# Performance work log

Measured on AMD Instinct MI355X. Metric: run time of the kernel, lower is better.

The kernel has to match this reference:

```python
import jax, jax.numpy as jnp
import numpy as np
import math
from functools import lru_cache

DIM = 64   # num_inputs
HID = 32   # hidden_dim
B = 1024
LOG2 = math.log(2.0)
LOG_2PI = math.log(2.0 * math.pi)


@lru_cache(maxsize=None)
def _masks(out_f, in_f, dim):
    ob, ib = out_f // dim, in_f // dim
    md = np.zeros((out_f, in_f), np.float32)
    mo = np.ones((out_f, in_f), np.float32)
    for i in range(dim):
        md[i * ob:(i + 1) * ob, i * ib:(i + 1) * ib] = 1.0
        mo[i * ob:(i + 1) * ob, i * ib:] = 0.0
    return jnp.asarray(md), jnp.asarray(mo)


def masked_weight(x, grad, W, dw, b, dim):
    # W: (out_f, in_f), dw: (out_f, 1), b: (out_f,)
    out_f, in_f = W.shape
    ob, ib = out_f // dim, in_f // dim
    md, mo = _masks(out_f, in_f, dim)
    w = jnp.exp(W) * md + W * mo                      # positive diag blocks, masked lower blocks
    wsn = jnp.sum(w * w, axis=-1, keepdims=True)      # (out_f, 1) weight-norm denom^2
    wn = jnp.exp(dw) * w / jnp.sqrt(wsn)              # weight-normalized matrix
    wpl = dw + W - 0.5 * jnp.log(wsn)                 # log of diag-block entries, (out_f, in_f)
    # extract diagonal blocks: (dim, ob, dim, ib) -> diag over block index -> (ob, ib, dim)
    blocks = jnp.diagonal(wpl.reshape(dim, ob, dim, ib), axis1=0, axis2=2)
    g = jnp.transpose(blocks, (2, 0, 1))              # (dim, ob, ib) == torch g per-sample
    out = x @ wn.T + b
    if grad is None:
        return out, jnp.broadcast_to(g[None], (x.shape[0],) + g.shape)
    # grad: (Bt, dim, a, c); log-domain block 'matmul' via logsumexp over shared axis a(=ib)
    comb = g[None, :, :, None, :] + jnp.swapaxes(grad, -1, -2)[:, :, None, :, :]  # (Bt,dim,ob,c,ib)
    return out, jax.nn.logsumexp(comb, axis=-1)       # (Bt, dim, ob, c)


def tanh_layer(x, grad):
    g = -2.0 * (x - LOG2 + jax.nn.softplus(-2.0 * x))
    return jnp.tanh(x), g.reshape(grad.shape) + grad


def bnaf_flow(x, p0, p1, p2, gate, dim):
    out, grad = masked_weight(x, None, *p0, dim)
    out, grad = tanh_layer(out, grad)
    out, grad = masked_weight(out, grad, *p1, dim)
    out, grad = tanh_layer(out, grad)
    out, grad = masked_weight(out, grad, *p2, dim)
    g = grad.reshape(grad.shape[0], dim)              # squeeze (B, dim, 1, 1) -> (B, dim)
    if gate is None:
        return out, jnp.sum(g, -1)
    s = jax.nn.sigmoid(gate)
    out = s * out + (1.0 - s) * x
    ldj = jnp.sum(jax.nn.softplus(g + gate) - jax.nn.softplus(gate), -1)
    return out, ldj


def _forward(x, params, gates):
    ldj = 0.0
    for f in range(3):
        gate = gates[f] if f < 2 else None
        x, l = bnaf_flow(x, params[f][0], params[f][1], params[f][2], gate, DIM)
        ldj = ldj + l
        if f < 2:
            x = x[:, ::-1]                            # Permutation('flip'), log-det 0
    log_p_y = jnp.sum(-0.5 * x * x - 0.5 * LOG_2PI, -1)
    return log_p_y + ldj                              # (B,)


def setup_inputs() -> dict:
    key = jax.random.key(0)
    ks = iter(jax.random.split(key, 64))
    d, dh = DIM, DIM * HID
    shapes = [(dh, d), (dh, dh), (d, dh)]
    inp = {"x": jax.random.normal(next(ks), (B, d), jnp.float32)}
    for f in range(3):
        for l, (o, i) in enumerate(shapes):
            inp[f"W{f}_{l}"] = 0.1 * jax.random.normal(next(ks), (o, i), jnp.float32)
            inp[f"dw{f}_{l}"] = jnp.log(jax.random.uniform(next(ks), (o, 1), jnp.float32, 0.1, 1.0))
            inp[f"b{f}_{l}"] = 0.01 * jax.random.normal(next(ks), (o,), jnp.float32)
    inp["gate0"] = jax.random.normal(next(ks), (1,), jnp.float32)
    inp["gate1"] = jax.random.normal(next(ks), (1,), jnp.float32)
    return inp


def reference(x, W0_0, dw0_0, b0_0, W0_1, dw0_1, b0_1, W0_2, dw0_2, b0_2,
              W1_0, dw1_0, b1_0, W1_1, dw1_1, b1_1, W1_2, dw1_2, b1_2,
              W2_0, dw2_0, b2_0, W2_1, dw2_1, b2_1, W2_2, dw2_2, b2_2,
              gate0, gate1):
    params = [
        [(W0_0, dw0_0, b0_0), (W0_1, dw0_1, b0_1), (W0_2, dw0_2, b0_2)],
        [(W1_0, dw1_0, b1_0), (W1_1, dw1_1, b1_1), (W1_2, dw1_2, b1_2)],
        [(W2_0, dw2_0, b2_0), (W2_1, dw2_1, b2_1), (W2_2, dw2_2, b2_2)],
    ]
    return _forward(x, params, (gate0, gate1))
```

## Files before the change

kernel.cpp:

```cpp
#include <hip/hip_runtime.h>
#include <hip/hip_bf16.h>
#include <math.h>


#define DIMN 64
#define BATCH 1024
#define HIDF 2048
#define SPLITK 4
#define NT2 32

typedef __attribute__((ext_vector_type(8))) short short8;
typedef __attribute__((ext_vector_type(4))) float floatx4;

__device__ __forceinline__ float softplusf_(float t) {
    return fmaxf(t, 0.f) + log1pf(__expf(-fabsf(t)));
}

__device__ __forceinline__ float bf2f(short v) {
    union { unsigned u; float f; } x;
    x.u = ((unsigned)(unsigned short)v) << 16;
    return x.f;
}

__device__ __forceinline__ void gl_lds16(const void* g, void* l) {
    __builtin_amdgcn_global_load_lds(
        (const __attribute__((address_space(1))) unsigned int*)g,
        (__attribute__((address_space(3))) unsigned int*)l, 16, 0, 0);
}

__device__ __forceinline__ void tanh_sech2_(float p, float& th, float& s2) {
    float t = __expf(-2.f * fabsf(p));
    float opt = 1.f + t;
    float inv = 1.f / opt;
    th = copysignf((1.f - t) * inv, p);
    s2 = 4.f * t * inv * inv;
}

template<int INF>
__device__ __forceinline__ void prep_row(
    const float* __restrict__ W, const float* __restrict__ dw,
    void* __restrict__ wn_out, float* __restrict__ eg,
    int r, int lane, int out_f, int ob, int ib, int transpose, int bf16out)
{
    constexpr int NI = INF / 64;
    int d = r / ob;
    int c0 = d * ib;
    int c1 = c0 + ib;
    const float* Wr = W + (size_t)r * INF;

    float vv[NI];
    float ss = 0.f;
#pragma unroll
    for (int i = 0; i < NI; ++i) {
        int c = lane + i * 64;
        float wraw = Wr[c];
        float wv = (c < c0) ? wraw : ((c < c1) ? __expf(wraw) : 0.f);
        vv[i] = wv;
        ss += wv * wv;
    }
    for (int off = 32; off > 0; off >>= 1) ss += __shfl_xor(ss, off, 64);

    float dwr = dw[r];
    float scale = __expf(dwr) / sqrtf(ss);
    float logt = dwr - 0.5f * __logf(ss);

#pragma unroll
    for (int i = 0; i < NI; ++i) {
        int c = lane + i * 64;
        float val = scale * vv[i];
        if (bf16out) {
            ((__hip_bfloat16*)wn_out)[(size_t)r * INF + c] = __float2bfloat16(val);
        } else if (transpose) {
            ((float*)wn_out)[(size_t)c * out_f + r] = val;
        } else {
            ((float*)wn_out)[(size_t)r * INF + c] = val;
        }
    }
    if (lane < ib) eg[(size_t)r * ib + lane] = __expf(logt + Wr[c0 + lane]);
}

struct PrepIn { const float *W0, *dw0, *W1, *dw1, *W2, *dw2; };

__global__ __launch_bounds__(64) void prep_mega(
    PrepIn p0, PrepIn p1, PrepIn p2,
    float* __restrict__ wn0T_all, float* __restrict__ eg0_all,
    __hip_bfloat16* __restrict__ wn1_all, float* __restrict__ e1_all,
    __hip_bfloat16* __restrict__ wn2b_all, float* __restrict__ e2_all)
{
    int blk = blockIdx.x;
    int lane = threadIdx.x;
    int f = blk / 4160;
    int rem = blk - f * 4160;
    PrepIn P = (f == 0) ? p0 : ((f == 1) ? p1 : p2);

    float* wn0T = wn0T_all + (size_t)f * DIMN * HIDF;
    float* eg0  = eg0_all  + (size_t)f * HIDF;
    __hip_bfloat16* wn1 = wn1_all + (size_t)f * HIDF * HIDF;
    float* e1   = e1_all   + (size_t)f * HIDF * 32;
    __hip_bfloat16* wn2b = wn2b_all + (size_t)f * DIMN * HIDF;
    float* e2   = e2_all   + (size_t)f * DIMN * 32;

    if (rem < HIDF) {
        prep_row<DIMN>(P.W0, P.dw0, wn0T, eg0, rem, lane, HIDF, 32, 1, 1, 0);
    } else if (rem < 2 * HIDF) {
        prep_row<HIDF>(P.W1, P.dw1, wn1, e1, rem - HIDF, lane, HIDF, 32, 32, 0, 1);
    } else {
        prep_row<HIDF>(P.W2, P.dw2, wn2b, e2, rem - 2 * HIDF, lane, DIMN, 1, 32, 0, 1);
    }
}

__global__ __launch_bounds__(256) void gemm0_act(
    const float* __restrict__ xin, const float* __restrict__ wn0T,
    const float* __restrict__ bias, const float* __restrict__ eg0,
    __hip_bfloat16* __restrict__ h0, __hip_bfloat16* __restrict__ g0e)
{
    __shared__ float xs[16][DIMN];
    int b0 = blockIdx.y * 16;
    {
        const float4* src = (const float4*)(xin + (size_t)b0 * DIMN);
        ((float4*)xs)[threadIdx.x] = src[threadIdx.x];
    }
    __syncthreads();
    int n = blockIdx.x * 256 + threadIdx.x;

    float acc[16];
#pragma unroll
    for (int j = 0; j < 16; ++j) acc[j] = 0.f;

#pragma unroll 4
    for (int c4 = 0; c4 < 16; ++c4) {
        int c = c4 * 4;
        float w0 = wn0T[(size_t)(c + 0) * HIDF + n];
        float w1 = wn0T[(size_t)(c + 1) * HIDF + n];
        float w2 = wn0T[(size_t)(c + 2) * HIDF + n];
        float w3 = wn0T[(size_t)(c + 3) * HIDF + n];
#pragma unroll
        for (int j = 0; j < 16; ++j) {
            float4 x4 = *(const float4*)&xs[j][c];
            acc[j] = fmaf(x4.x, w0, acc[j]);
            acc[j] = fmaf(x4.y, w1, acc[j]);
            acc[j] = fmaf(x4.z, w2, acc[j]);
            acc[j] = fmaf(x4.w, w3, acc[j]);
        }
    }
    float bv = bias[n], egv = eg0[n];
#pragma unroll
    for (int j = 0; j < 16; ++j) {
        float p = acc[j] + bv;
        float th, s2;
        tanh_sech2_(p, th, s2);
        size_t idx = (size_t)(b0 + j) * HIDF + n;
        h0[idx] = __float2bfloat16(th);
        g0e[idx] = __float2bfloat16(egv * s2);
    }
}

__constant__ unsigned char G1_JN[40] = {
    3,4,5,6,7,7,8,8,9,9,10,10,11,11,11,12,12,12,13,13,13,14,14,14,
    15,15,15,15, 2,6,10,14, 1,5,9,13, 0,4,8,12 };
__constant__ unsigned char G1_KZ[40] = {
    0,0,0,0,0,1,0,1,0,1, 0, 1, 0, 1, 2, 0, 1, 2, 0, 1, 2, 0, 1, 2,
     0, 1, 2, 3, 0,1, 2, 3, 0,1,2,3, 0,1,2,3 };

#define G1BK 64
__global__ __launch_bounds__(256) void gemm1_part(
    const __hip_bfloat16* __restrict__ A, const __hip_bfloat16* __restrict__ B,
    __hip_bfloat16* __restrict__ part)
{
    const int K = HIDF, N = HIDF;
    int pr = blockIdx.x >> 3;
    int my = blockIdx.x & 7;
    int jn = G1_JN[pr];
    int kz = G1_KZ[pr];
    int kbase = kz * (K / SPLITK);
    int kend = (jn + 1) * 128 - kbase;
    if (kend > K / SPLITK) kend = K / SPLITK;

    __shared__ short As[128 * 64];
    __shared__ short Bs[128 * 64];
    int tid = threadIdx.x;
    int lane = tid & 63;
    int wave = tid >> 6;
    int n0 = jn * 128;
    int m0 = my * 128;
    int wr = wave >> 1;
    int wc = wave & 1;

    int rf = lane & 15;
    int q = lane >> 4;

    const char* agp[4];
    const char* bgp[4];
    char* alds[4];
    char* blds[4];
#pragma unroll
    for (int s = 0; s < 4; ++s) {
        int c = tid + s * 256;
        int row = c >> 3;
        int kc = (c & 7) ^ (row & 7);
        agp[s] = (const char*)A + ((size_t)(m0 + row) * K + kbase) * 2 + kc * 16;
        bgp[s] = (const char*)B + ((size_t)(n0 + row) * K + kbase) * 2 + kc * 16;
        alds[s] = (char*)As + c * 16;
        blds[s] = (char*)Bs + c * 16;
    }

    floatx4 acc[4][4];
#pragma unroll
    for (int i = 0; i < 4; ++i)
#pragma unroll
        for (int j = 0; j < 4; ++j) acc[i][j] = (floatx4){0.f, 0.f, 0.f, 0.f};

    int rowA0 = wr * 64 + rf;
    int rowB0 = wc * 64 + rf;

    for (int k0 = 0; k0 < kend; k0 += G1BK) {
        size_t kb = (size_t)k0 * 2;
        __syncthreads();
#pragma unroll
        for (int s = 0; s < 4; ++s) {
            gl_lds16(agp[s] + kb, alds[s]);
            gl_lds16(bgp[s] + kb, blds[s]);
        }
        __syncthreads();

#pragma unroll
        for (int s = 0; s < 2; ++s) {
            short8 af[4], bfv[4];
#pragma unroll
            for (int i = 0; i < 4; ++i) {
                int row = rowA0 + i * 16;
                af[i] = *(const short8*)&As[row * 64 + (((s * 4 + q) ^ (row & 7)) * 8)];
            }
#pragma unroll
            for (int j = 0; j < 4; ++j) {
                int row = rowB0 + j * 16;
                bfv[j] = *(const short8*)&Bs[row * 64 + (((s * 4 + q) ^ (row & 7)) * 8)];
            }
#pragma unroll
            for (int i = 0; i < 4; ++i)
#pragma unroll
                for (int j = 0; j < 4; ++j)
                    acc[i][j] = __builtin_amdgcn_mfma_f32_16x16x32_bf16(af[i], bfv[j], acc[i][j], 0, 0, 0);
        }
    }

    __hip_bfloat16* pk = part + (size_t)kz * BATCH * HIDF;
    int col = lane & 15;
    int rq = (lane >> 4) * 4;
#pragma unroll
    for (int i = 0; i < 4; ++i) {
#pragma unroll
        for (int j = 0; j < 4; ++j) {
            int n = n0 + wc * 64 + j * 16 + col;
#pragma unroll
            for (int r = 0; r < 4; ++r) {
                int m = m0 + wr * 64 + i * 16 + rq + r;
                pk[(size_t)m * N + n] = __float2bfloat16(acc[i][j][r]);
            }
        }
    }
}

__global__ __launch_bounds__(256) void act_grad_gemm2(
    const __hip_bfloat16* __restrict__ part, const float* __restrict__ bias,
    const float* __restrict__ e1, const __hip_bfloat16* __restrict__ g0e,
    const __hip_bfloat16* __restrict__ wn2b,
    __hip_bfloat16* __restrict__ grad1e, float* __restrict__ out2p)
{
    __shared__ char smem[17408 + 8704 + 8192];
    float* g0s = (float*)smem;
    short* h1s = (short*)(smem + 17408);
    short* Bs2 = (short*)(smem + 17408 + 8704);

    int tid = threadIdx.x;
    int lane = tid & 63;
    int wave = tid >> 6;
    int bx = blockIdx.x;
    int n0 = bx * 64;
    int b0 = blockIdx.y * 64;
    int np = (bx >> 3) + 1;

    {
        int c0c = tid, c1c = tid + 256;
        int r0 = c0c >> 3, k0c = (c0c & 7) ^ (r0 & 7);
        int r1 = c1c >> 3, k1c = (c1c & 7) ^ (r1 & 7);
        gl_lds16((const char*)wn2b + ((size_t)r0 * HIDF + n0) * 2 + k0c * 16,
                 (char*)Bs2 + c0c * 16);
        gl_lds16((const char*)wn2b + ((size_t)r1 * HIDF + n0) * 2 + k1c * 16,
                 (char*)Bs2 + c1c * 16);
    }

    for (int s = tid; s < 512; s += 256) {
        int row = s >> 3, c8 = s & 7;
        short8 v = *(const short8*)((const short*)g0e +
                                    (size_t)(b0 + row) * HIDF + n0 + c8 * 8);
        float4 lo = { bf2f(v[0]), bf2f(v[1]), bf2f(v[2]), bf2f(v[3]) };
        float4 hi = { bf2f(v[4]), bf2f(v[5]), bf2f(v[6]), bf2f(v[7]) };
        *(float4*)&g0s[row * 68 + c8 * 8] = lo;
        *(float4*)&g0s[row * 68 + c8 * 8 + 4] = hi;
    }

    int g = tid >> 6;
    int nl = tid & 63;
    int n = n0 + nl;

    float4 er[8];
    const float4* e1r = (const float4*)(e1 + (size_t)n * 32);
#pragma unroll
    for (int qq = 0; qq < 8; ++qq) er[qq] = e1r[qq];

    float bv = bias[n];
    int kb2 = nl & 32;
    const __hip_bfloat16* pp0 = part;
    const __hip_bfloat16* pp1 = (np > 1) ? part + (size_t)1 * BATCH * HIDF : part;
    const __hip_bfloat16* pp2 = (np > 2) ? part + (size_t)2 * BATCH * HIDF : part;
    const __hip_bfloat16* pp3 = (np > 3) ? part + (size_t)3 * BATCH * HIDF : part;
    float m1 = (np > 1) ? 1.f : 0.f;
    float m2 = (np > 2) ? 1.f : 0.f;
    float m3 = (np > 3) ? 1.f : 0.f;

    __syncthreads();

#pragma unroll
    for (int t = 0; t < 16; ++t) {
        int bl = g * 16 + t;
        int b = b0 + bl;
        size_t idx = (size_t)b * HIDF + n;
        float l0 = __bfloat162float(pp0[idx]);
        float l1 = __bfloat162float(pp1[idx]);
        float l2 = __bfloat162float(pp2[idx]);
        float l3 = __bfloat162float(pp3[idx]);
        float pre = bv + l0;
        pre = fmaf(m1, l1, pre);
        pre = fmaf(m2, l2, pre);
        pre = fmaf(m3, l3, pre);
        float th, s2;
        tanh_sech2_(pre, th, s2);
        const float* g0row = &g0s[bl * 68 + kb2];
        float dot = 0.f;
#pragma unroll
        for (int qq = 0; qq < 8; ++qq) {
            float4 gv = *(const float4*)&g0row[qq * 4];
            dot = fmaf(gv.x, er[qq].x, dot);
            dot = fmaf(gv.y, er[qq].y, dot);
            dot = fmaf(gv.z, er[qq].z, dot);
            dot = fmaf(gv.w, er[qq].w, dot);
        }
        __hip_bfloat16 thb = __float2bfloat16(th);
        h1s[bl * 68 + nl] = *(const short*)&thb;
        grad1e[idx] = __float2bfloat16(dot * s2);
    }
    __syncthreads();

    int rf = lane & 15;
    int q = lane >> 4;
    floatx4 acc2[4];
#pragma unroll
    for (int j = 0; j < 4; ++j) acc2[j] = (floatx4){0.f, 0.f, 0.f, 0.f};

#pragma unroll
    for (int s = 0; s < 2; ++s) {
        int rowa = wave * 16 + rf;
        short8 af = *(const short8*)&h1s[rowa * 68 + s * 32 + q * 8];
#pragma unroll
        for (int j = 0; j < 4; ++j) {
            int rowb = j * 16 + rf;
            int cp = (s * 4 + q) ^ (rowb & 7);
            short8 bfv = *(const short8*)&Bs2[rowb * 64 + cp * 8];
            acc2[j] = __builtin_amdgcn_mfma_f32_16x16x32_bf16(af, bfv, acc2[j], 0, 0, 0);
        }
    }

    float* outk = out2p + (size_t)bx * BATCH * DIMN;
    int col = lane & 15;
    int rq = (lane >> 4) * 4;
#pragma unroll
    for (int j = 0; j < 4; ++j) {
#pragma unroll
        for (int r = 0; r < 4; ++r) {
            int m = b0 + wave * 16 + rq + r;
            outk[(size_t)m * DIMN + j * 16 + col] = acc2[j][r];
        }
    }
}

__global__ __launch_bounds__(256) void tail_trans(
    const float* __restrict__ out2p, const float* __restrict__ b2,
    const float* __restrict__ e2, const __hip_bfloat16* __restrict__ grad1e,
    const float* __restrict__ x_cur, const float* __restrict__ gate,
    float* __restrict__ x_next, float* __restrict__ ldj, int accum_ldj)
{
    int tid = threadIdx.x;
    int b = blockIdx.x * 4 + (tid >> 6);
    int n = tid & 63;

    float o = b2[n];
#pragma unroll
    for (int p = 0; p < NT2; ++p)
        o += out2p[(size_t)p * BATCH * DIMN + (size_t)b * DIMN + n];

    float gt = gate[0];
    float sg = 1.f / (1.f + __expf(-gt));
    float xo = sg * o + (1.f - sg) * x_cur[(size_t)b * DIMN + n];
    x_next[(size_t)b * DIMN + (63 - n)] = xo;

    const short8* gr = (const short8*)((const short*)grad1e + (size_t)b * HIDF + n * 32);
    const float4* gc = (const float4*)(e2 + n * 32);
    float s = 0.f;
#pragma unroll
    for (int q = 0; q < 4; ++q) {
        short8 a8 = gr[q];
        float4 c0 = gc[2 * q], c1 = gc[2 * q + 1];
        s = fmaf(bf2f(a8[0]), c0.x, s);
        s = fmaf(bf2f(a8[1]), c0.y, s);
        s = fmaf(bf2f(a8[2]), c0.z, s);
        s = fmaf(bf2f(a8[3]), c0.w, s);
        s = fmaf(bf2f(a8[4]), c1.x, s);
        s = fmaf(bf2f(a8[5]), c1.y, s);
        s = fmaf(bf2f(a8[6]), c1.z, s);
        s = fmaf(bf2f(a8[7]), c1.w, s);
    }
    float gF = __logf(fmaxf(s, 1e-45f));
    float contrib = softplusf_(gF + gt) - softplusf_(gt);
    for (int off = 32; off > 0; off >>= 1) contrib += __shfl_xor(contrib, off, 64);
    if (n == 0) ldj[b] = accum_ldj ? (ldj[b] + contrib) : contrib;
}

__global__ __launch_bounds__(256) void tail_final(
    const float* __restrict__ out2p, const float* __restrict__ b2,
    const float* __restrict__ e2, const __hip_bfloat16* __restrict__ grad1e,
    const float* __restrict__ ldj, float* __restrict__ out)
{
    int tid = threadIdx.x;
    int b = blockIdx.x * 4 + (tid >> 6);
    int n = tid & 63;

    float o = b2[n];
#pragma unroll
    for (int p = 0; p < NT2; ++p)
        o += out2p[(size_t)p * BATCH * DIMN + (size_t)b * DIMN + n];

    const short8* gr = (const short8*)((const short*)grad1e + (size_t)b * HIDF + n * 32);
    const float4* gc = (const float4*)(e2 + n * 32);
    float s = 0.f;
#pragma unroll
    for (int q = 0; q < 4; ++q) {
        short8 a8 = gr[q];
        float4 c0 = gc[2 * q], c1 = gc[2 * q + 1];
        s = fmaf(bf2f(a8[0]), c0.x, s);
        s = fmaf(bf2f(a8[1]), c0.y, s);
        s = fmaf(bf2f(a8[2]), c0.z, s);
        s = fmaf(bf2f(a8[3]), c0.w, s);
        s = fmaf(bf2f(a8[4]), c1.x, s);
        s = fmaf(bf2f(a8[5]), c1.y, s);
        s = fmaf(bf2f(a8[6]), c1.z, s);
        s = fmaf(bf2f(a8[7]), c1.w, s);
    }
    float gF = __logf(fmaxf(s, 1e-45f));

    float contrib = gF - 0.5f * o * o - 0.91893853320467274f;
    for (int off = 32; off > 0; off >>= 1) contrib += __shfl_xor(contrib, off, 64);
    if (n == 0) out[b] = ldj[b] + contrib;
}

extern "C" void kernel_launch(void* const* d_in, const int* in_sizes, int n_in,
                              void* d_out, int out_size, void* d_ws, size_t ws_size,
                              hipStream_t stream)
{
    (void)in_sizes; (void)n_in; (void)out_size; (void)ws_size;

    const float* x = (const float*)d_in[0];
    const float* gates[2] = { (const float*)d_in[28], (const float*)d_in[29] };

    char* ws = (char*)d_ws;
    size_t ofs = 0;
    auto alloc = [&](size_t bytes) { char* p = ws + ofs; ofs += (bytes + 255) & ~(size_t)255; return p; };

    __hip_bfloat16* wn1_all  = (__hip_bfloat16*)alloc((size_t)3 * HIDF * HIDF * 2);
    __hip_bfloat16* wn2b_all = (__hip_bfloat16*)alloc((size_t)3 * DIMN * HIDF * 2);
    float* wn0T_all = (float*)alloc((size_t)3 * DIMN * HIDF * 4);
    float* eg0_all  = (float*)alloc((size_t)3 * HIDF * 4);
    float* e1_all   = (float*)alloc((size_t)3 * HIDF * 32 * 4);
    float* e2_all   = (float*)alloc((size_t)3 * DIMN * 32 * 4);
    __hip_bfloat16* h0   = (__hip_bfloat16*)alloc((size_t)BATCH * HIDF * 2);
    __hip_bfloat16* part = (__hip_bfloat16*)alloc((size_t)SPLITK * BATCH * HIDF * 2);
    __hip_bfloat16* g0e    = (__hip_bfloat16*)alloc((size_t)BATCH * HIDF * 2);
    __hip_bfloat16* grad1e = (__hip_bfloat16*)alloc((size_t)BATCH * HIDF * 2);
    float* out2p  = (float*)alloc((size_t)NT2 * BATCH * DIMN * 4);
    float* x1     = (float*)alloc((size_t)BATCH * DIMN * 4);
    float* x2     = (float*)alloc((size_t)BATCH * DIMN * 4);
    float* ldj    = (float*)alloc(BATCH * 4);
    float* outp   = (float*)d_out;

    auto W = [&](int f, int i) { return (const float*)d_in[1 + f * 9 + i]; };

    PrepIn p0 = { W(0,0), W(0,1), W(0,3), W(0,4), W(0,6), W(0,7) };
    PrepIn p1 = { W(1,0), W(1,1), W(1,3), W(1,4), W(1,6), W(1,7) };
    PrepIn p2 = { W(2,0), W(2,1), W(2,3), W(2,4), W(2,6), W(2,7) };

    prep_mega<<<dim3(3 * 4160), dim3(64), 0, stream>>>(
        p0, p1, p2, wn0T_all, eg0_all, wn1_all, e1_all, wn2b_all, e2_all);

    gemm0_act<<<dim3(8, BATCH / 16), dim3(256), 0, stream>>>(
        x, wn0T_all, W(0,2), eg0_all, h0, g0e);

    const float* xcur = x;
    float* xnexts[2] = { x1, x2 };

    for (int f = 0; f < 3; ++f) {
        size_t fo1 = (size_t)f * HIDF * HIDF;
        size_t fo2 = (size_t)f * DIMN * HIDF;

        gemm1_part<<<dim3(320), dim3(256), 0, stream>>>(
            h0, wn1_all + fo1, part);

        act_grad_gemm2<<<dim3(HIDF / 64, BATCH / 64), dim3(256), 0, stream>>>(
            part, W(f,5), e1_all + (size_t)f * HIDF * 32, g0e,
            wn2b_all + fo2, grad1e, out2p);

        if (f < 2) {
            tail_trans<<<dim3(BATCH / 4), dim3(256), 0, stream>>>(
                out2p, W(f,8), e2_all + (size_t)f * DIMN * 32, grad1e,
                xcur, gates[f], xnexts[f], ldj, f);

            gemm0_act<<<dim3(8, BATCH / 16), dim3(256), 0, stream>>>(
                xnexts[f], wn0T_all + (size_t)(f + 1) * DIMN * HIDF, W(f + 1, 2),
                eg0_all + (size_t)(f + 1) * HIDF, h0, g0e);

            xcur = xnexts[f];
        } else {
            tail_final<<<dim3(BATCH / 4), dim3(256), 0, stream>>>(
                out2p, W(2,8), e2_all + (size_t)2 * DIMN * 32, grad1e, ldj, outp);
        }
    }
}
```

Baseline: 291.4 us.

## Double-buffer LDS loads in gemm1 and fuse next-flow gemm0 into tail kernel

gemm1_part now keeps two LDS stages, so the global-to-LDS copy for the next K tile is issued while MFMAs run on the current tile, and only one barrier is needed per iteration. Separately, the tail kernel for flows 0 and 1 now also computes the next flow's first layer (x @ wn0T, tanh, gradient) from an LDS copy of the new x, which removes the separate gemm0_act launch. LDS per gemm1 block doubles to 64 KB, which may lower occupancy. The fused gemm0 runs on only 4 batch rows per block and re-reads the full wn0T in each of 256 blocks, so it reuses weights far less than the old 16-row kernel.

```diff
diff --git a/kernel.cpp b/kernel.cpp
--- a/kernel.cpp
+++ b/kernel.cpp
@@ -11,6 +11,7 @@
 
 typedef __attribute__((ext_vector_type(8))) short short8;
 typedef __attribute__((ext_vector_type(4))) float floatx4;
+typedef __hip_bfloat16 bf16;
 
 __device__ __forceinline__ float softplusf_(float t) {
     return fmaxf(t, 0.f) + log1pf(__expf(-fabsf(t)));
@@ -69,7 +70,7 @@
         int c = lane + i * 64;
         float val = scale * vv[i];
         if (bf16out) {
-            ((__hip_bfloat16*)wn_out)[(size_t)r * INF + c] = __float2bfloat16(val);
+            ((bf16*)wn_out)[(size_t)r * INF + c] = __float2bfloat16(val);
         } else if (transpose) {
             ((float*)wn_out)[(size_t)c * out_f + r] = val;
         } else {
@@ -84,8 +85,8 @@
 __global__ __launch_bounds__(64) void prep_mega(
     PrepIn p0, PrepIn p1, PrepIn p2,
     float* __restrict__ wn0T_all, float* __restrict__ eg0_all,
-    __hip_bfloat16* __restrict__ wn1_all, float* __restrict__ e1_all,
-    __hip_bfloat16* __restrict__ wn2b_all, float* __restrict__ e2_all)
+    bf16* __restrict__ wn1_all, float* __restrict__ e1_all,
+    bf16* __restrict__ wn2b_all, float* __restrict__ e2_all)
 {
     int blk = blockIdx.x;
     int lane = threadIdx.x;
@@ -95,9 +96,9 @@
 
     float* wn0T = wn0T_all + (size_t)f * DIMN * HIDF;
     float* eg0  = eg0_all  + (size_t)f * HIDF;
-    __hip_bfloat16* wn1 = wn1_all + (size_t)f * HIDF * HIDF;
+    bf16* wn1   = wn1_all + (size_t)f * HIDF * HIDF;
     float* e1   = e1_all   + (size_t)f * HIDF * 32;
-    __hip_bfloat16* wn2b = wn2b_all + (size_t)f * DIMN * HIDF;
+    bf16* wn2b  = wn2b_all + (size_t)f * DIMN * HIDF;
     float* e2   = e2_all   + (size_t)f * DIMN * 32;
 
     if (rem < HIDF) {
@@ -112,7 +113,7 @@
 __global__ __launch_bounds__(256) void gemm0_act(
     const float* __restrict__ xin, const float* __restrict__ wn0T,
     const float* __restrict__ bias, const float* __restrict__ eg0,
-    __hip_bfloat16* __restrict__ h0, __hip_bfloat16* __restrict__ g0e)
+    bf16* __restrict__ h0, bf16* __restrict__ g0e)
 {
     __shared__ float xs[16][DIMN];
     int b0 = blockIdx.y * 16;
@@ -164,9 +165,10 @@
 
 #define G1BK 64
 __global__ __launch_bounds__(256) void gemm1_part(
-    const __hip_bfloat16* __restrict__ A, const __hip_bfloat16* __restrict__ B,
-    __hip_bfloat16* __restrict__ part)
-{
+    const bf16* __restrict__ A, const bf16* __restrict__ B,
+    bf16* __restrict__ part)
+{
+    __shared__ __align__(16) char smem_[65536];
     const int K = HIDF, N = HIDF;
     int pr = blockIdx.x >> 3;
     int my = blockIdx.x & 7;
@@ -176,8 +178,6 @@
     int kend = (jn + 1) * 128 - kbase;
     if (kend > K / SPLITK) kend = K / SPLITK;
 
-    __shared__ short As[128 * 64];
-    __shared__ short Bs[128 * 64];
     int tid = threadIdx.x;
     int lane = tid & 63;
     int wave = tid >> 6;
@@ -185,14 +185,12 @@
     int m0 = my * 128;
     int wr = wave >> 1;
     int wc = wave & 1;
-
     int rf = lane & 15;
     int q = lane >> 4;
 
     const char* agp[4];
     const char* bgp[4];
-    char* alds[4];
-    char* blds[4];
+    int lofs[4];
 #pragma unroll
     for (int s = 0; s < 4; ++s) {
         int c = tid + s * 256;
@@ -200,8 +198,7 @@
         int kc = (c & 7) ^ (row & 7);
         agp[s] = (const char*)A + ((size_t)(m0 + row) * K + kbase) * 2 + kc * 16;
         bgp[s] = (const char*)B + ((size_t)(n0 + row) * K + kbase) * 2 + kc * 16;
-        alds[s] = (char*)As + c * 16;
-        blds[s] = (char*)Bs + c * 16;
+        lofs[s] = c * 16;
     }
 
     floatx4 acc[4][4];
@@ -213,16 +210,31 @@
     int rowA0 = wr * 64 + rf;
     int rowB0 = wc * 64 + rf;
 
+    {
+        char* base = smem_;
+#pragma unroll
+        for (int s = 0; s < 4; ++s) {
+            gl_lds16(agp[s], base + lofs[s]);
+            gl_lds16(bgp[s], base + 16384 + lofs[s]);
+        }
+    }
+    __syncthreads();
+
+    int cur = 0;
     for (int k0 = 0; k0 < kend; k0 += G1BK) {
-        size_t kb = (size_t)k0 * 2;
-        __syncthreads();
-#pragma unroll
-        for (int s = 0; s < 4; ++s) {
-            gl_lds16(agp[s] + kb, alds[s]);
-            gl_lds16(bgp[s] + kb, blds[s]);
-        }
-        __syncthreads();
-
+        int nk = k0 + G1BK;
+        if (nk < kend) {
+            size_t kb = (size_t)nk * 2;
+            char* base = smem_ + (cur ^ 1) * 32768;
+#pragma unroll
+            for (int s = 0; s < 4; ++s) {
+                gl_lds16(agp[s] + kb, base + lofs[s]);
+                gl_lds16(bgp[s] + kb, base + 16384 + lofs[s]);
+            }
+        }
+
+        const short* As = (const short*)(smem_ + cur * 32768);
+        const short* Bs = (const short*)(smem_ + cur * 32768 + 16384);
 #pragma unroll
         for (int s = 0; s < 2; ++s) {
             short8 af[4], bfv[4];
@@ -242,9 +254,11 @@
                 for (int j = 0; j < 4; ++j)
                     acc[i][j] = __builtin_amdgcn_mfma_f32_16x16x32_bf16(af[i], bfv[j], acc[i][j], 0, 0, 0);
         }
-    }
-
-    __hip_bfloat16* pk = part + (size_t)kz * BATCH * HIDF;
+        __syncthreads();
+        cur ^= 1;
+    }
+
+    bf16* pk = part + (size_t)kz * BATCH * HIDF;
     int col = lane & 15;
     int rq = (lane >> 4) * 4;
 #pragma unroll
@@ -262,10 +276,10 @@
 }
 
 __global__ __launch_bounds__(256) void act_grad_gemm2(
-    const __hip_bfloat16* __restrict__ part, const float* __restrict__ bias,
-    const float* __restrict__ e1, const __hip_bfloat16* __restrict__ g0e,
-    const __hip_bfloat16* __restrict__ wn2b,
-    __hip_bfloat16* __restrict__ grad1e, float* __restrict__ out2p)
+    const bf16* __restrict__ part, const float* __restrict__ bias,
+    const float* __restrict__ e1, const bf16* __restrict__ g0e,
+    const bf16* __restrict__ wn2b,
+    bf16* __restrict__ grad1e, float* __restrict__ out2p)
 {
     __shared__ char smem[17408 + 8704 + 8192];
     float* g0s = (float*)smem;
@@ -311,10 +325,10 @@
 
     float bv = bias[n];
     int kb2 = nl & 32;
-    const __hip_bfloat16* pp0 = part;
-    const __hip_bfloat16* pp1 = (np > 1) ? part + (size_t)1 * BATCH * HIDF : part;
-    const __hip_bfloat16* pp2 = (np > 2) ? part + (size_t)2 * BATCH * HIDF : part;
-    const __hip_bfloat16* pp3 = (np > 3) ? part + (size_t)3 * BATCH * HIDF : part;
+    const bf16* pp0 = part;
+    const bf16* pp1 = (np > 1) ? part + (size_t)1 * BATCH * HIDF : part;
+    const bf16* pp2 = (np > 2) ? part + (size_t)2 * BATCH * HIDF : part;
+    const bf16* pp3 = (np > 3) ? part + (size_t)3 * BATCH * HIDF : part;
     float m1 = (np > 1) ? 1.f : 0.f;
     float m2 = (np > 2) ? 1.f : 0.f;
     float m3 = (np > 3) ? 1.f : 0.f;
@@ -346,7 +360,7 @@
             dot = fmaf(gv.z, er[qq].z, dot);
             dot = fmaf(gv.w, er[qq].w, dot);
         }
-        __hip_bfloat16 thb = __float2bfloat16(th);
+        bf16 thb = __float2bfloat16(th);
         h1s[bl * 68 + nl] = *(const short*)&thb;
         grad1e[idx] = __float2bfloat16(dot * s2);
     }
@@ -384,14 +398,19 @@
     }
 }
 
-__global__ __launch_bounds__(256) void tail_trans(
+__global__ __launch_bounds__(256) void tail_gemm0(
     const float* __restrict__ out2p, const float* __restrict__ b2,
-    const float* __restrict__ e2, const __hip_bfloat16* __restrict__ grad1e,
+    const float* __restrict__ e2, const bf16* __restrict__ grad1e,
     const float* __restrict__ x_cur, const float* __restrict__ gate,
-    float* __restrict__ x_next, float* __restrict__ ldj, int accum_ldj)
-{
+    float* __restrict__ x_next, float* __restrict__ ldj, int accum_ldj,
+    const float* __restrict__ wn0T_n, const float* __restrict__ bias_n,
+    const float* __restrict__ eg0_n,
+    bf16* __restrict__ h0, bf16* __restrict__ g0e)
+{
+    __shared__ float xs[4][DIMN];
     int tid = threadIdx.x;
-    int b = blockIdx.x * 4 + (tid >> 6);
+    int row = tid >> 6;
+    int b = blockIdx.x * 4 + row;
     int n = tid & 63;
 
     float o = b2[n];
@@ -403,6 +422,7 @@
     float sg = 1.f / (1.f + __expf(-gt));
     float xo = sg * o + (1.f - sg) * x_cur[(size_t)b * DIMN + n];
     x_next[(size_t)b * DIMN + (63 - n)] = xo;
+    xs[row][63 - n] = xo;
 
     const short8* gr = (const short8*)((const short*)grad1e + (size_t)b * HIDF + n * 32);
     const float4* gc = (const float4*)(e2 + n * 32);
@@ -424,11 +444,42 @@
     float contrib = softplusf_(gF + gt) - softplusf_(gt);
     for (int off = 32; off > 0; off >>= 1) contrib += __shfl_xor(contrib, off, 64);
     if (n == 0) ldj[b] = accum_ldj ? (ldj[b] + contrib) : contrib;
+
+    __syncthreads();
+
+    int b0r = blockIdx.x * 4;
+#pragma unroll 1
+    for (int i = 0; i < 8; ++i) {
+        int n2 = tid + (i << 8);
+        float a0 = 0.f, a1 = 0.f, a2 = 0.f, a3 = 0.f;
+#pragma unroll 8
+        for (int c = 0; c < 64; ++c) {
+            float w = wn0T_n[(size_t)c * HIDF + n2];
+            a0 = fmaf(xs[0][c], w, a0);
+            a1 = fmaf(xs[1][c], w, a1);
+            a2 = fmaf(xs[2][c], w, a2);
+            a3 = fmaf(xs[3][c], w, a3);
+        }
+        float bv = bias_n[n2], egv = eg0_n[n2];
+        float th, s2;
+        tanh_sech2_(a0 + bv, th, s2);
+        h0[(size_t)(b0r + 0) * HIDF + n2] = __float2bfloat16(th);
+        g0e[(size_t)(b0r + 0) * HIDF + n2] = __float2bfloat16(egv * s2);
+        tanh_sech2_(a1 + bv, th, s2);
+        h0[(size_t)(b0r + 1) * HIDF + n2] = __float2bfloat16(th);
+        g0e[(size_t)(b0r + 1) * HIDF + n2] = __float2bfloat16(egv * s2);
+        tanh_sech2_(a2 + bv, th, s2);
+        h0[(size_t)(b0r + 2) * HIDF + n2] = __float2bfloat16(th);
+        g0e[(size_t)(b0r + 2) * HIDF + n2] = __float2bfloat16(egv * s2);
+        tanh_sech2_(a3 + bv, th, s2);
+        h0[(size_t)(b0r + 3) * HIDF + n2] = __float2bfloat16(th);
+        g0e[(size_t)(b0r + 3) * HIDF + n2] = __float2bfloat16(egv * s2);
+    }
 }
 
 __global__ __launch_bounds__(256) void tail_final(
     const float* __restrict__ out2p, const float* __restrict__ b2,
-    const float* __restrict__ e2, const __hip_bfloat16* __restrict__ grad1e,
+    const float* __restrict__ e2, const bf16* __restrict__ grad1e,
     const float* __restrict__ ldj, float* __restrict__ out)
 {
     int tid = threadIdx.x;
@@ -476,16 +527,16 @@
     size_t ofs = 0;
     auto alloc = [&](size_t bytes) { char* p = ws + ofs; ofs += (bytes + 255) & ~(size_t)255; return p; };
 
-    __hip_bfloat16* wn1_all  = (__hip_bfloat16*)alloc((size_t)3 * HIDF * HIDF * 2);
-    __hip_bfloat16* wn2b_all = (__hip_bfloat16*)alloc((size_t)3 * DIMN * HIDF * 2);
+    bf16* wn1_all  = (bf16*)alloc((size_t)3 * HIDF * HIDF * 2);
+    bf16* wn2b_all = (bf16*)alloc((size_t)3 * DIMN * HIDF * 2);
     float* wn0T_all = (float*)alloc((size_t)3 * DIMN * HIDF * 4);
     float* eg0_all  = (float*)alloc((size_t)3 * HIDF * 4);
     float* e1_all   = (float*)alloc((size_t)3 * HIDF * 32 * 4);
     float* e2_all   = (float*)alloc((size_t)3 * DIMN * 32 * 4);
-    __hip_bfloat16* h0   = (__hip_bfloat16*)alloc((size_t)BATCH * HIDF * 2);
-    __hip_bfloat16* part = (__hip_bfloat16*)alloc((size_t)SPLITK * BATCH * HIDF * 2);
-    __hip_bfloat16* g0e    = (__hip_bfloat16*)alloc((size_t)BATCH * HIDF * 2);
-    __hip_bfloat16* grad1e = (__hip_bfloat16*)alloc((size_t)BATCH * HIDF * 2);
+    bf16* h0   = (bf16*)alloc((size_t)BATCH * HIDF * 2);
+    bf16* part = (bf16*)alloc((size_t)SPLITK * BATCH * HIDF * 2);
+    bf16* g0e    = (bf16*)alloc((size_t)BATCH * HIDF * 2);
+    bf16* grad1e = (bf16*)alloc((size_t)BATCH * HIDF * 2);
     float* out2p  = (float*)alloc((size_t)NT2 * BATCH * DIMN * 4);
     float* x1     = (float*)alloc((size_t)BATCH * DIMN * 4);
     float* x2     = (float*)alloc((size_t)BATCH * DIMN * 4);
@@ -519,14 +570,11 @@
             wn2b_all + fo2, grad1e, out2p);
 
         if (f < 2) {
-            tail_trans<<<dim3(BATCH / 4), dim3(256), 0, stream>>>(
+            tail_gemm0<<<dim3(BATCH / 4), dim3(256), 0, stream>>>(
                 out2p, W(f,8), e2_all + (size_t)f * DIMN * 32, grad1e,
-                xcur, gates[f], xnexts[f], ldj, f);
-
-            gemm0_act<<<dim3(8, BATCH / 16), dim3(256), 0, stream>>>(
-                xnexts[f], wn0T_all + (size_t)(f + 1) * DIMN * HIDF, W(f + 1, 2),
+                xcur, gates[f], xnexts[f], ldj, f,
+                wn0T_all + (size_t)(f + 1) * DIMN * HIDF, W(f + 1, 2),
                 eg0_all + (size_t)(f + 1) * HIDF, h0, g0e);
-
             xcur = xnexts[f];
         } else {
             tail_final<<<dim3(BATCH / 4), dim3(256), 0, stream>>>(
```

Result: slower. 308.0 us (+5.7%).
